# Kernel tuning notes

Measured on AMD Instinct MI355X. Metric: run time of the kernel, lower is better.

The kernel has to match this reference:

```python
import jax, jax.numpy as jnp
import numpy as np

N_NODES = 50000
N_EDGES = 800000
D_IN = 128
D_OUT = 128  # hidden_size == output_size == 128


def setup_inputs() -> dict:
    key = jax.random.key(0)
    k_x, k_src, k_dst, k_w1, k_w2 = jax.random.split(key, 5)
    x = jax.random.normal(k_x, (N_NODES, D_IN), dtype=jnp.float32)
    src = jax.random.randint(k_src, (N_EDGES,), 0, N_NODES)
    dst = jax.random.randint(k_dst, (N_EDGES,), 0, N_NODES)
    # SGConv fc weight (torch Linear layout: [out, in]) and bias
    w_conv = jax.random.normal(k_w1, (D_OUT, D_IN), dtype=jnp.float32) / np.sqrt(D_IN)
    b_conv = jnp.zeros((D_OUT,), dtype=jnp.float32)
    # trailing Linear(hidden_size=128 -> output_size=128)
    w_lin = jax.random.normal(k_w2, (D_OUT, D_OUT), dtype=jnp.float32) / np.sqrt(D_OUT)
    b_lin = jnp.zeros((D_OUT,), dtype=jnp.float32)
    return {"x": x, "src": src, "dst": dst,
            "w_conv": w_conv, "b_conv": b_conv,
            "w_lin": w_lin, "b_lin": b_lin}


def reference(x, src, dst, w_conv, b_conv, w_lin, b_lin):
    n = x.shape[0]
    # symmetric normalization by in-degree (DGL SGConv, k=1 hop)
    deg = jax.ops.segment_sum(jnp.ones_like(dst, dtype=x.dtype), dst, num_segments=n)
    norm = jax.lax.rsqrt(jnp.clip(deg, 1.0))[:, None]  # [N,1]
    h = x * norm                                        # D^{-1/2} X
    h = jax.ops.segment_sum(h[src], dst, num_segments=n)  # A (D^{-1/2} X), spmm via gather+scatter-add
    h = h * norm                                        # D^{-1/2} A D^{-1/2} X
    h = jnp.maximum(h @ w_conv.T + b_conv, 0.0)         # SGConv fc + relu
    return jnp.maximum(h @ w_lin.T + b_lin, 0.0)        # Linear + relu
```

## Files before the change

### kernel.cpp

```cpp
#include <hip/hip_runtime.h>

#define N_NODES 50000
#define N_EDGES 800000
#define D 128
#define ROWS 16
#define BCAP 255
#define LCAP 64
#define ESC_BLOCKS 3125
#define XCONV_BLOCKS 3125
#define NORM_BLOCKS 196
#define WSPLIT_BLOCKS 128
#define XB_OFF 200064
#define WHI_OFF 13000064
#define WS_NEEDED 13131136ull

typedef int   v4i __attribute__((ext_vector_type(4)));
typedef float v4f __attribute__((ext_vector_type(4)));


__device__ __forceinline__ unsigned short bf_rne(float v) {
    unsigned u = __float_as_uint(v);
    u += 0x7FFFu + ((u >> 16) & 1u);
    return (unsigned short)(u >> 16);
}
__device__ __forceinline__ float bf_up(unsigned short h) {
    return __uint_as_float((unsigned)h << 16);
}
__device__ __forceinline__ void split_pack(float a, float b, unsigned& hw, unsigned& lw) {
    unsigned short ha = bf_rne(a);
    unsigned short hb = bf_rne(b);
    unsigned short la = bf_rne(a - bf_up(ha));
    unsigned short lb = bf_rne(b - bf_up(hb));
    hw = (unsigned)ha | ((unsigned)hb << 16);
    lw = (unsigned)la | ((unsigned)lb << 16);
}
__device__ __forceinline__ unsigned pack2(float a, float b) {
    return (unsigned)bf_rne(a) | ((unsigned)bf_rne(b) << 16);
}

__global__ void scatter_kernel(const int* __restrict__ src, const int* __restrict__ dst,
                               int* __restrict__ deg, unsigned short* outSlots,
                               const float* __restrict__ x, unsigned short* __restrict__ xb,
                               const float* __restrict__ w1, const float* __restrict__ w2,
                               unsigned short* __restrict__ whi1, unsigned short* __restrict__ wlo1,
                               unsigned short* __restrict__ whi2, unsigned short* __restrict__ wlo2) {
    int b = blockIdx.x, t = threadIdx.x;
    if (b < ESC_BLOCKS) {
        int e = b * 256 + t;
        int s = src[e], d = dst[e];
        int p = atomicAdd(&deg[d], 1);
        if (p < BCAP) outSlots[(size_t)d * 256 + p] = (unsigned short)s;
    } else if (b < ESC_BLOCKS + XCONV_BLOCKS) {
        int i = (b - ESC_BLOCKS) * 256 + t;
        float4 a = *(const float4*)(x + (size_t)8 * i);
        float4 c = *(const float4*)(x + (size_t)8 * i + 4);
        uint4 o;
        o.x = pack2(a.x, a.y);
        o.y = pack2(a.z, a.w);
        o.z = pack2(c.x, c.y);
        o.w = pack2(c.z, c.w);
        *(uint4*)(xb + (size_t)8 * i) = o;
    } else {
        int m = (b - ESC_BLOCKS - XCONV_BLOCKS) * 256 + t;
        int sel = m >> 14;
        int j = m & 16383;
        float v = sel ? w2[j] : w1[j];
        unsigned short h = bf_rne(v);
        unsigned short lo = bf_rne(v - bf_up(h));
        if (sel) { whi2[j] = h; wlo2[j] = lo; }
        else     { whi1[j] = h; wlo1[j] = lo; }
    }
}

__global__ void prep_kernel(const int* __restrict__ deg, float* __restrict__ normArr,
                            const float* __restrict__ w1, const float* __restrict__ w2,
                            unsigned short* __restrict__ whi1, unsigned short* __restrict__ wlo1,
                            unsigned short* __restrict__ whi2, unsigned short* __restrict__ wlo2) {
    int b = blockIdx.x, t = threadIdx.x;
    if (b < NORM_BLOCKS) {
        int n = b * 256 + t;
        if (n < N_NODES)
            normArr[n] = rsqrtf(fmaxf((float)deg[n], 1.0f));
    } else {
        int m = (b - NORM_BLOCKS) * 256 + t;
        int sel = m >> 14;
        int j = m & 16383;
        float v = sel ? w2[j] : w1[j];
        unsigned short h = bf_rne(v);
        unsigned short lo = bf_rne(v - bf_up(h));
        if (sel) { whi2[j] = h; wlo2[j] = lo; }
        else     { whi1[j] = h; wlo1[j] = lo; }
    }
}

#define MLP_BODY                                                               \
    int wv = t >> 6;                                                           \
    int cb = wv << 5;                                                          \
    int l15 = l & 15;                                                          \
    int kq = l >> 4;                                                           \
    const char* phiA = (const char*)&Ahi[l15][0];                              \
    const char* ploA = (const char*)&Alo[l15][0];                              \
    v4i ahi[4], alo[4];                                                        \
_Pragma("unroll")                                                              \
    for (int kt = 0; kt < 4; ++kt) {                                           \
        int off = ((((kt << 2) | kq) ^ l15) << 4);                             \
        ahi[kt] = *(const v4i*)(phiA + off);                                   \
        alo[kt] = *(const v4i*)(ploA + off);                                   \
    }                                                                          \
    __syncthreads();                                                           \
_Pragma("unroll")                                                              \
    for (int ct = 0; ct < 2; ++ct) {                                           \
        int c = cb + (ct << 4) + l15;                                          \
        float bv = b1[c];                                                      \
        v4f acc = {bv, bv, bv, bv};                                            \
        const unsigned short* wh = whi1 + c * D + (kq << 3);                   \
        const unsigned short* wl = wlo1 + c * D + (kq << 3);                   \
_Pragma("unroll")                                                              \
        for (int kt = 0; kt < 4; ++kt) {                                       \
            v4i bh = *(const v4i*)(wh + (kt << 5));                            \
            v4i bl = *(const v4i*)(wl + (kt << 5));                            \
            asm volatile("v_mfma_f32_16x16x32_bf16 %0, %1, %2, %0" : "+v"(acc) : "v"(ahi[kt]), "v"(bh)); \
            asm volatile("v_mfma_f32_16x16x32_bf16 %0, %1, %2, %0" : "+v"(acc) : "v"(alo[kt]), "v"(bh)); \
            asm volatile("v_mfma_f32_16x16x32_bf16 %0, %1, %2, %0" : "+v"(acc) : "v"(ahi[kt]), "v"(bl)); \
        }                                                                      \
        asm volatile("s_nop 7\n\ts_nop 7" : "+v"(acc));                        \
_Pragma("unroll")                                                              \
        for (int r = 0; r < 4; ++r) {                                          \
            float v = fmaxf(acc[r], 0.0f);                                     \
            unsigned short hv = bf_rne(v);                                     \
            unsigned short lv = bf_rne(v - bf_up(hv));                         \
            int ro = (kq << 2) + r;                                            \
            int byte = (2 * c) ^ ((ro & 15) << 4);                             \
            *(unsigned short*)((char*)&Ahi[ro][0] + byte) = hv;                \
            *(unsigned short*)((char*)&Alo[ro][0] + byte) = lv;                \
        }                                                                      \
    }                                                                          \
    __syncthreads();                                                           \
_Pragma("unroll")                                                              \
    for (int kt = 0; kt < 4; ++kt) {                                           \
        int off = ((((kt << 2) | kq) ^ l15) << 4);                             \
        ahi[kt] = *(const v4i*)(phiA + off);                                   \
        alo[kt] = *(const v4i*)(ploA + off);                                   \
    }                                                                          \
_Pragma("unroll")                                                              \
    for (int ct = 0; ct < 2; ++ct) {                                           \
        int c = cb + (ct << 4) + l15;                                          \
        float bv = b2[c];                                                      \
        v4f acc = {bv, bv, bv, bv};                                            \
        const unsigned short* wh = whi2 + c * D + (kq << 3);                   \
        const unsigned short* wl = wlo2 + c * D + (kq << 3);                   \
_Pragma("unroll")                                                              \
        for (int kt = 0; kt < 4; ++kt) {                                       \
            v4i bh = *(const v4i*)(wh + (kt << 5));                            \
            v4i bl = *(const v4i*)(wl + (kt << 5));                            \
            asm volatile("v_mfma_f32_16x16x32_bf16 %0, %1, %2, %0" : "+v"(acc) : "v"(ahi[kt]), "v"(bh)); \
            asm volatile("v_mfma_f32_16x16x32_bf16 %0, %1, %2, %0" : "+v"(acc) : "v"(alo[kt]), "v"(bh)); \
            asm volatile("v_mfma_f32_16x16x32_bf16 %0, %1, %2, %0" : "+v"(acc) : "v"(ahi[kt]), "v"(bl)); \
        }                                                                      \
        asm volatile("s_nop 7\n\ts_nop 7" : "+v"(acc));                        \
_Pragma("unroll")                                                              \
        for (int r = 0; r < 4; ++r) {                                          \
            int ro = row_base + (kq << 2) + r;                                 \
            if (ro < N_NODES)                                                  \
                io[(size_t)ro * D + c] = fmaxf(acc[r], 0.0f);                  \
        }                                                                      \
    }

__global__ __launch_bounds__(256) void fused_gather_mlp_bf16(
    const unsigned short* __restrict__ xb,
    const unsigned short* slotsIn,
    const int* __restrict__ deg,
    float* io,
    const unsigned short* __restrict__ whi1, const unsigned short* __restrict__ wlo1,
    const float* __restrict__ b1,
    const unsigned short* __restrict__ whi2, const unsigned short* __restrict__ wlo2,
    const float* __restrict__ b2) {
    __shared__ __align__(16) unsigned short Ahi[ROWS][D];
    __shared__ __align__(16) unsigned short Alo[ROWS][D];
    __shared__ unsigned short colsL[ROWS][LCAP];
    __shared__ float ncolL[ROWS][LCAP];
    __shared__ int degL[ROWS];
    __shared__ int nextRow;
    int row_base = blockIdx.x * ROWS;
    int t = threadIdx.x;
    int tx = t & 31;
    int l = t & 63;

    if (t < ROWS) degL[t] = deg[row_base + t];
    if (t == ROWS) nextRow = 0;
    __syncthreads();

    for (int e2 = t; e2 < ROWS * LCAP; e2 += 256) {
        int r = e2 >> 6;
        int j = e2 & (LCAP - 1);
        if (j < degL[r]) {
            int s = slotsIn[(size_t)(row_base + r) * 256 + j];
            colsL[r][j] = (unsigned short)s;
            ncolL[r][j] = rsqrtf(fmaxf((float)deg[s], 1.0f));
        } else {
            colsL[r][j] = 0;
            ncolL[r][j] = 0.f;
        }
    }
    __syncthreads();

    for (;;) {
        int rr;
        if (tx == 0) rr = atomicAdd(&nextRow, 1);
        rr = __shfl(rr, l & 32);
        if (rr >= ROWS) break;
        int dr = degL[rr];
        float nr = rsqrtf(fmaxf((float)dr, 1.0f));
        float4 acc = make_float4(0.f, 0.f, 0.f, 0.f);
        int jend = min(dr, LCAP);
        for (int j = 0; j < jend; j += 8) {
            int s0 = colsL[rr][j + 0], s1 = colsL[rr][j + 1], s2 = colsL[rr][j + 2], s3 = colsL[rr][j + 3];
            int s4 = colsL[rr][j + 4], s5 = colsL[rr][j + 5], s6 = colsL[rr][j + 6], s7 = colsL[rr][j + 7];
            float n0 = ncolL[rr][j + 0], n1 = ncolL[rr][j + 1], n2 = ncolL[rr][j + 2], n3 = ncolL[rr][j + 3];
            float n4 = ncolL[rr][j + 4], n5 = ncolL[rr][j + 5], n6 = ncolL[rr][j + 6], n7 = ncolL[rr][j + 7];
            uint2 v0 = *(const uint2*)(xb + (size_t)s0 * D + 4 * tx);
            uint2 v1 = *(const uint2*)(xb + (size_t)s1 * D + 4 * tx);
            uint2 v2 = *(const uint2*)(xb + (size_t)s2 * D + 4 * tx);
            uint2 v3 = *(const uint2*)(xb + (size_t)s3 * D + 4 * tx);
            uint2 v4 = *(const uint2*)(xb + (size_t)s4 * D + 4 * tx);
            uint2 v5 = *(const uint2*)(xb + (size_t)s5 * D + 4 * tx);
            uint2 v6 = *(const uint2*)(xb + (size_t)s6 * D + 4 * tx);
            uint2 v7 = *(const uint2*)(xb + (size_t)s7 * D + 4 * tx);
            acc.x += __uint_as_float(v0.x << 16) * n0 + __uint_as_float(v1.x << 16) * n1
                   + __uint_as_float(v2.x << 16) * n2 + __uint_as_float(v3.x << 16) * n3
                   + __uint_as_float(v4.x << 16) * n4 + __uint_as_float(v5.x << 16) * n5
                   + __uint_as_float(v6.x << 16) * n6 + __uint_as_float(v7.x << 16) * n7;
            acc.y += __uint_as_float(v0.x & 0xffff0000u) * n0 + __uint_as_float(v1.x & 0xffff0000u) * n1
                   + __uint_as_float(v2.x & 0xffff0000u) * n2 + __uint_as_float(v3.x & 0xffff0000u) * n3
                   + __uint_as_float(v4.x & 0xffff0000u) * n4 + __uint_as_float(v5.x & 0xffff0000u) * n5
                   + __uint_as_float(v6.x & 0xffff0000u) * n6 + __uint_as_float(v7.x & 0xffff0000u) * n7;
            acc.z += __uint_as_float(v0.y << 16) * n0 + __uint_as_float(v1.y << 16) * n1
                   + __uint_as_float(v2.y << 16) * n2 + __uint_as_float(v3.y << 16) * n3
                   + __uint_as_float(v4.y << 16) * n4 + __uint_as_float(v5.y << 16) * n5
                   + __uint_as_float(v6.y << 16) * n6 + __uint_as_float(v7.y << 16) * n7;
            acc.w += __uint_as_float(v0.y & 0xffff0000u) * n0 + __uint_as_float(v1.y & 0xffff0000u) * n1
                   + __uint_as_float(v2.y & 0xffff0000u) * n2 + __uint_as_float(v3.y & 0xffff0000u) * n3
                   + __uint_as_float(v4.y & 0xffff0000u) * n4 + __uint_as_float(v5.y & 0xffff0000u) * n5
                   + __uint_as_float(v6.y & 0xffff0000u) * n6 + __uint_as_float(v7.y & 0xffff0000u) * n7;
        }
        if (dr > LCAP) {
            int je = min(dr, BCAP);
            for (int j = LCAP; j < je; ++j) {
                int s = slotsIn[(size_t)(row_base + rr) * 256 + j];
                float nv = rsqrtf(fmaxf((float)deg[s], 1.0f));
                uint2 v = *(const uint2*)(xb + (size_t)s * D + 4 * tx);
                acc.x += __uint_as_float(v.x << 16) * nv;
                acc.y += __uint_as_float(v.x & 0xffff0000u) * nv;
                acc.z += __uint_as_float(v.y << 16) * nv;
                acc.w += __uint_as_float(v.y & 0xffff0000u) * nv;
            }
        }
        acc.x *= nr; acc.y *= nr; acc.z *= nr; acc.w *= nr;
        unsigned hw0, lw0, hw1, lw1;
        split_pack(acc.x, acc.y, hw0, lw0);
        split_pack(acc.z, acc.w, hw1, lw1);
        int byte = (8 * tx) ^ ((rr & 15) << 4);
        *(uint2*)((char*)&Ahi[rr][0] + byte) = make_uint2(hw0, hw1);
        *(uint2*)((char*)&Alo[rr][0] + byte) = make_uint2(lw0, lw1);
    }
    __syncthreads();

    MLP_BODY
}

__global__ __launch_bounds__(256) void fused_gather_mlp_f32(
    const float* __restrict__ x,
    const unsigned short* slotsIn,
    const float* __restrict__ normArr, const int* __restrict__ deg,
    float* io,
    const unsigned short* __restrict__ whi1, const unsigned short* __restrict__ wlo1,
    const float* __restrict__ b1,
    const unsigned short* __restrict__ whi2, const unsigned short* __restrict__ wlo2,
    const float* __restrict__ b2) {
    __shared__ __align__(16) unsigned short Ahi[ROWS][D];
    __shared__ __align__(16) unsigned short Alo[ROWS][D];
    __shared__ unsigned short colsL[ROWS][LCAP];
    __shared__ float ncolL[ROWS][LCAP];
    __shared__ int degL[ROWS];
    __shared__ int nextRow;
    int row_base = blockIdx.x * ROWS;
    int t = threadIdx.x;
    int tx = t & 31;
    int l = t & 63;

    if (t < ROWS) degL[t] = deg[row_base + t];
    if (t == ROWS) nextRow = 0;
    __syncthreads();

    for (int e2 = t; e2 < ROWS * LCAP; e2 += 256) {
        int r = e2 >> 6;
        int j = e2 & (LCAP - 1);
        if (j < degL[r]) {
            int s = slotsIn[(size_t)(row_base + r) * 256 + j];
            colsL[r][j] = (unsigned short)s;
            ncolL[r][j] = normArr[s];
        } else {
            colsL[r][j] = 0;
            ncolL[r][j] = 0.f;
        }
    }
    __syncthreads();

    for (;;) {
        int rr;
        if (tx == 0) rr = atomicAdd(&nextRow, 1);
        rr = __shfl(rr, l & 32);
        if (rr >= ROWS) break;
        int dr = degL[rr];
        float nr = rsqrtf(fmaxf((float)dr, 1.0f));
        float4 acc = make_float4(0.f, 0.f, 0.f, 0.f);
        int jend = min(dr, LCAP);
        for (int j = 0; j < jend; j += 8) {
            int s0 = colsL[rr][j + 0], s1 = colsL[rr][j + 1], s2 = colsL[rr][j + 2], s3 = colsL[rr][j + 3];
            int s4 = colsL[rr][j + 4], s5 = colsL[rr][j + 5], s6 = colsL[rr][j + 6], s7 = colsL[rr][j + 7];
            float n0 = ncolL[rr][j + 0], n1 = ncolL[rr][j + 1], n2 = ncolL[rr][j + 2], n3 = ncolL[rr][j + 3];
            float n4 = ncolL[rr][j + 4], n5 = ncolL[rr][j + 5], n6 = ncolL[rr][j + 6], n7 = ncolL[rr][j + 7];
            float4 x0 = *(const float4*)(x + (size_t)s0 * D + 4 * tx);
            float4 x1 = *(const float4*)(x + (size_t)s1 * D + 4 * tx);
            float4 x2 = *(const float4*)(x + (size_t)s2 * D + 4 * tx);
            float4 x3 = *(const float4*)(x + (size_t)s3 * D + 4 * tx);
            float4 x4 = *(const float4*)(x + (size_t)s4 * D + 4 * tx);
            float4 x5 = *(const float4*)(x + (size_t)s5 * D + 4 * tx);
            float4 x6 = *(const float4*)(x + (size_t)s6 * D + 4 * tx);
            float4 x7 = *(const float4*)(x + (size_t)s7 * D + 4 * tx);
            acc.x += x0.x * n0 + x1.x * n1 + x2.x * n2 + x3.x * n3
                   + x4.x * n4 + x5.x * n5 + x6.x * n6 + x7.x * n7;
            acc.y += x0.y * n0 + x1.y * n1 + x2.y * n2 + x3.y * n3
                   + x4.y * n4 + x5.y * n5 + x6.y * n6 + x7.y * n7;
            acc.z += x0.z * n0 + x1.z * n1 + x2.z * n2 + x3.z * n3
                   + x4.z * n4 + x5.z * n5 + x6.z * n6 + x7.z * n7;
            acc.w += x0.w * n0 + x1.w * n1 + x2.w * n2 + x3.w * n3
                   + x4.w * n4 + x5.w * n5 + x6.w * n6 + x7.w * n7;
        }
        if (dr > LCAP) {
            int je = min(dr, BCAP);
            for (int j = LCAP; j < je; ++j) {
                int s = slotsIn[(size_t)(row_base + rr) * 256 + j];
                float nv = normArr[s];
                float4 xv = *(const float4*)(x + (size_t)s * D + 4 * tx);
                acc.x += xv.x * nv; acc.y += xv.y * nv;
                acc.z += xv.z * nv; acc.w += xv.w * nv;
            }
        }
        acc.x *= nr; acc.y *= nr; acc.z *= nr; acc.w *= nr;
        unsigned hw0, lw0, hw1, lw1;
        split_pack(acc.x, acc.y, hw0, lw0);
        split_pack(acc.z, acc.w, hw1, lw1);
        int byte = (8 * tx) ^ ((rr & 15) << 4);
        *(uint2*)((char*)&Ahi[rr][0] + byte) = make_uint2(hw0, hw1);
        *(uint2*)((char*)&Alo[rr][0] + byte) = make_uint2(lw0, lw1);
    }
    __syncthreads();

    MLP_BODY
}

extern "C" void kernel_launch(void* const* d_in, const int* in_sizes, int n_in,
                              void* d_out, int out_size, void* d_ws, size_t ws_size,
                              hipStream_t stream) {
    const float* x      = (const float*)d_in[0];
    const int*   src    = (const int*)d_in[1];
    int*         dstbuf = (int*)d_in[2];
    const float* w_conv = (const float*)d_in[3];
    const float* b_conv = (const float*)d_in[4];
    const float* w_lin  = (const float*)d_in[5];
    const float* b_lin  = (const float*)d_in[6];

    int* deg = (int*)d_ws;
    unsigned short* xb = (unsigned short*)((char*)d_ws + XB_OFF);
    const bool big = ws_size >= WS_NEEDED;

    hipMemsetAsync(deg, 0, (size_t)N_NODES * sizeof(int), stream);
    if (big) {
        unsigned short* whi1 = (unsigned short*)((char*)d_ws + WHI_OFF);
        unsigned short* wlo1 = (unsigned short*)((char*)d_ws + WHI_OFF + 32768);
        unsigned short* whi2 = (unsigned short*)((char*)d_ws + WHI_OFF + 65536);
        unsigned short* wlo2 = (unsigned short*)((char*)d_ws + WHI_OFF + 98304);
        scatter_kernel<<<ESC_BLOCKS + XCONV_BLOCKS + WSPLIT_BLOCKS, 256, 0, stream>>>(
            src, (const int*)dstbuf, deg, (unsigned short*)d_out, x, xb,
            w_conv, w_lin, whi1, wlo1, whi2, wlo2);
        fused_gather_mlp_bf16<<<N_NODES / ROWS, 256, 0, stream>>>(
            xb, (const unsigned short*)d_out, deg, (float*)d_out,
            whi1, wlo1, b_conv, whi2, wlo2, b_lin);
    } else {
        float* normArr = (float*)dstbuf;
        unsigned short* whi1 = (unsigned short*)((char*)dstbuf + 200000);
        unsigned short* wlo1 = (unsigned short*)((char*)dstbuf + 232768);
        unsigned short* whi2 = (unsigned short*)((char*)dstbuf + 265536);
        unsigned short* wlo2 = (unsigned short*)((char*)dstbuf + 298304);
        scatter_kernel<<<ESC_BLOCKS, 256, 0, stream>>>(
            src, (const int*)dstbuf, deg, (unsigned short*)d_out, x, xb,
            w_conv, w_lin, whi1, wlo1, whi2, wlo2);
        prep_kernel<<<NORM_BLOCKS + WSPLIT_BLOCKS, 256, 0, stream>>>(
            deg, normArr, w_conv, w_lin, whi1, wlo1, whi2, wlo2);
        fused_gather_mlp_f32<<<N_NODES / ROWS, 256, 0, stream>>>(
            x, (const unsigned short*)d_out, normArr, deg, (float*)d_out,
            whi1, wlo1, b_conv, whi2, wlo2, b_lin);
    }
}
```

Baseline: 204.6 us.

## Replicate degree counters eightfold to reduce atomic contention in edge scatter

Adds a new path, used when the workspace is large enough, that splits each node's degree counter into 8 sub-counters chosen by edge index. Each sub-counter owns a 32-slot region of the node's slot list, which cuts atomic contention on hot destination nodes. The fused gather kernel then sums the sub-counters to get true degrees and compacts the slot lists into shared memory. The costs are an 8x larger memset, extra loads of 8 ints per neighbor for normalization, and more complex slot compaction. Sub-bucket overflow past 32 could also drop edges on skewed inputs.

```diff
diff --git a/kernel.cpp b/kernel.cpp
--- a/kernel.cpp
+++ b/kernel.cpp
@@ -5,6 +5,7 @@
 #define D 128
 #define ROWS 16
 #define BCAP 255
+#define RCAP 32
 #define LCAP 64
 #define ESC_BLOCKS 3125
 #define XCONV_BLOCKS 3125
@@ -12,7 +13,10 @@
 #define WSPLIT_BLOCKS 128
 #define XB_OFF 200064
 #define WHI_OFF 13000064
-#define WS_NEEDED 13131136ull
+#define WS1_NEEDED 13131136ull
+#define XB2_OFF 1600064
+#define WHI2_OFF 14400064
+#define WS2_NEEDED 14531136ull
 
 typedef int   v4i __attribute__((ext_vector_type(4)));
 typedef float v4f __attribute__((ext_vector_type(4)));
@@ -36,6 +40,41 @@
 }
 __device__ __forceinline__ unsigned pack2(float a, float b) {
     return (unsigned)bf_rne(a) | ((unsigned)bf_rne(b) << 16);
+}
+
+__global__ void scatter8_kernel(const int* __restrict__ src, const int* __restrict__ dst,
+                                int* __restrict__ deg8, unsigned short* outSlots,
+                                const float* __restrict__ x, unsigned short* __restrict__ xb,
+                                const float* __restrict__ w1, const float* __restrict__ w2,
+                                unsigned short* __restrict__ whi1, unsigned short* __restrict__ wlo1,
+                                unsigned short* __restrict__ whi2, unsigned short* __restrict__ wlo2) {
+    int b = blockIdx.x, t = threadIdx.x;
+    if (b < ESC_BLOCKS) {
+        int e = b * 256 + t;
+        int s = src[e], d = dst[e];
+        int k = e & 7;
+        int p = atomicAdd(&deg8[(size_t)d * 8 + k], 1);
+        if (p < RCAP) outSlots[(size_t)d * 256 + k * RCAP + p] = (unsigned short)s;
+    } else if (b < ESC_BLOCKS + XCONV_BLOCKS) {
+        int i = (b - ESC_BLOCKS) * 256 + t;
+        float4 a = *(const float4*)(x + (size_t)8 * i);
+        float4 c = *(const float4*)(x + (size_t)8 * i + 4);
+        uint4 o;
+        o.x = pack2(a.x, a.y);
+        o.y = pack2(a.z, a.w);
+        o.z = pack2(c.x, c.y);
+        o.w = pack2(c.z, c.w);
+        *(uint4*)(xb + (size_t)8 * i) = o;
+    } else {
+        int m = (b - ESC_BLOCKS - XCONV_BLOCKS) * 256 + t;
+        int sel = m >> 14;
+        int j = m & 16383;
+        float v = sel ? w2[j] : w1[j];
+        unsigned short h = bf_rne(v);
+        unsigned short lo = bf_rne(v - bf_up(h));
+        if (sel) { whi2[j] = h; wlo2[j] = lo; }
+        else     { whi1[j] = h; wlo1[j] = lo; }
+    }
 }
 
 __global__ void scatter_kernel(const int* __restrict__ src, const int* __restrict__ dst,
@@ -166,6 +205,139 @@
         }                                                                      \
     }
 
+#define BF16_CHUNK8(RR, J)                                                     \
+    {                                                                          \
+        int s0 = colsL[RR][J + 0], s1 = colsL[RR][J + 1], s2 = colsL[RR][J + 2], s3 = colsL[RR][J + 3]; \
+        int s4 = colsL[RR][J + 4], s5 = colsL[RR][J + 5], s6 = colsL[RR][J + 6], s7 = colsL[RR][J + 7]; \
+        float n0 = ncolL[RR][J + 0], n1 = ncolL[RR][J + 1], n2 = ncolL[RR][J + 2], n3 = ncolL[RR][J + 3]; \
+        float n4 = ncolL[RR][J + 4], n5 = ncolL[RR][J + 5], n6 = ncolL[RR][J + 6], n7 = ncolL[RR][J + 7]; \
+        uint2 v0 = *(const uint2*)(xb + (size_t)s0 * D + 4 * tx);              \
+        uint2 v1 = *(const uint2*)(xb + (size_t)s1 * D + 4 * tx);              \
+        uint2 v2 = *(const uint2*)(xb + (size_t)s2 * D + 4 * tx);              \
+        uint2 v3 = *(const uint2*)(xb + (size_t)s3 * D + 4 * tx);              \
+        uint2 v4 = *(const uint2*)(xb + (size_t)s4 * D + 4 * tx);              \
+        uint2 v5 = *(const uint2*)(xb + (size_t)s5 * D + 4 * tx);              \
+        uint2 v6 = *(const uint2*)(xb + (size_t)s6 * D + 4 * tx);              \
+        uint2 v7 = *(const uint2*)(xb + (size_t)s7 * D + 4 * tx);              \
+        acc.x += __uint_as_float(v0.x << 16) * n0 + __uint_as_float(v1.x << 16) * n1 \
+               + __uint_as_float(v2.x << 16) * n2 + __uint_as_float(v3.x << 16) * n3 \
+               + __uint_as_float(v4.x << 16) * n4 + __uint_as_float(v5.x << 16) * n5 \
+               + __uint_as_float(v6.x << 16) * n6 + __uint_as_float(v7.x << 16) * n7; \
+        acc.y += __uint_as_float(v0.x & 0xffff0000u) * n0 + __uint_as_float(v1.x & 0xffff0000u) * n1 \
+               + __uint_as_float(v2.x & 0xffff0000u) * n2 + __uint_as_float(v3.x & 0xffff0000u) * n3 \
+               + __uint_as_float(v4.x & 0xffff0000u) * n4 + __uint_as_float(v5.x & 0xffff0000u) * n5 \
+               + __uint_as_float(v6.x & 0xffff0000u) * n6 + __uint_as_float(v7.x & 0xffff0000u) * n7; \
+        acc.z += __uint_as_float(v0.y << 16) * n0 + __uint_as_float(v1.y << 16) * n1 \
+               + __uint_as_float(v2.y << 16) * n2 + __uint_as_float(v3.y << 16) * n3 \
+               + __uint_as_float(v4.y << 16) * n4 + __uint_as_float(v5.y << 16) * n5 \
+               + __uint_as_float(v6.y << 16) * n6 + __uint_as_float(v7.y << 16) * n7; \
+        acc.w += __uint_as_float(v0.y & 0xffff0000u) * n0 + __uint_as_float(v1.y & 0xffff0000u) * n1 \
+               + __uint_as_float(v2.y & 0xffff0000u) * n2 + __uint_as_float(v3.y & 0xffff0000u) * n3 \
+               + __uint_as_float(v4.y & 0xffff0000u) * n4 + __uint_as_float(v5.y & 0xffff0000u) * n5 \
+               + __uint_as_float(v6.y & 0xffff0000u) * n6 + __uint_as_float(v7.y & 0xffff0000u) * n7; \
+    }
+
+__global__ __launch_bounds__(256) void fused_gather_mlp_rep(
+    const unsigned short* __restrict__ xb,
+    const unsigned short* slotsIn,
+    const int* __restrict__ deg8,
+    float* io,
+    const unsigned short* __restrict__ whi1, const unsigned short* __restrict__ wlo1,
+    const float* __restrict__ b1,
+    const unsigned short* __restrict__ whi2, const unsigned short* __restrict__ wlo2,
+    const float* __restrict__ b2) {
+    __shared__ __align__(16) unsigned short Ahi[ROWS][D];
+    __shared__ __align__(16) unsigned short Alo[ROWS][D];
+    __shared__ unsigned short colsL[ROWS][LCAP];
+    __shared__ float ncolL[ROWS][LCAP];
+    __shared__ unsigned char cntL[ROWS][8];
+    __shared__ unsigned char offL[ROWS][8];
+    __shared__ int dcapL[ROWS];
+    __shared__ float nrL[ROWS];
+    __shared__ int nextRow;
+    int row_base = blockIdx.x * ROWS;
+    int t = threadIdx.x;
+    int tx = t & 31;
+    int l = t & 63;
+
+    for (int i = t; i < ROWS * LCAP; i += 256) {
+        colsL[i >> 6][i & (LCAP - 1)] = 0;
+        ncolL[i >> 6][i & (LCAP - 1)] = 0.f;
+    }
+    if (t == 0) nextRow = 0;
+    if (t < ROWS) {
+        const int4* p = (const int4*)(deg8 + (size_t)(row_base + t) * 8);
+        int4 a = p[0], b = p[1];
+        int cc[8] = {a.x, a.y, a.z, a.w, b.x, b.y, b.z, b.w};
+        int tru = 0, off = 0;
+#pragma unroll
+        for (int k = 0; k < 8; ++k) {
+            tru += cc[k];
+            int c = min(cc[k], RCAP);
+            cntL[t][k] = (unsigned char)c;
+            offL[t][k] = (unsigned char)off;
+            off += c;
+        }
+        dcapL[t] = off;
+        nrL[t] = rsqrtf(fmaxf((float)tru, 1.0f));
+    }
+    __syncthreads();
+
+    for (int e2 = t; e2 < ROWS * 256; e2 += 256) {
+        int r = e2 >> 8, slot = e2 & 255, k = slot >> 5, j = slot & 31;
+        if (j < (int)cntL[r][k]) {
+            int s = slotsIn[(size_t)(row_base + r) * 256 + slot];
+            int idx = (int)offL[r][k] + j;
+            if (idx < LCAP) {
+                colsL[r][idx] = (unsigned short)s;
+                const int4* q = (const int4*)(deg8 + (size_t)s * 8);
+                int4 a = q[0], b = q[1];
+                int sd = a.x + a.y + a.z + a.w + b.x + b.y + b.z + b.w;
+                ncolL[r][idx] = rsqrtf(fmaxf((float)sd, 1.0f));
+            }
+        }
+    }
+    __syncthreads();
+
+    for (;;) {
+        int rr;
+        if (tx == 0) rr = atomicAdd(&nextRow, 1);
+        rr = __shfl(rr, l & 32);
+        if (rr >= ROWS) break;
+        float nr = nrL[rr];
+        float4 acc = make_float4(0.f, 0.f, 0.f, 0.f);
+        int jend = min(dcapL[rr], LCAP);
+        for (int j = 0; j < jend; j += 8) BF16_CHUNK8(rr, j)
+        if (dcapL[rr] > LCAP) {
+            for (int slot = 0; slot < 256; ++slot) {
+                int k = slot >> 5, j = slot & 31;
+                if (j < (int)cntL[rr][k] && (int)offL[rr][k] + j >= LCAP) {
+                    int s = slotsIn[(size_t)(row_base + rr) * 256 + slot];
+                    const int4* q = (const int4*)(deg8 + (size_t)s * 8);
+                    int4 a = q[0], b = q[1];
+                    int sd = a.x + a.y + a.z + a.w + b.x + b.y + b.z + b.w;
+                    float nv = rsqrtf(fmaxf((float)sd, 1.0f));
+                    uint2 v = *(const uint2*)(xb + (size_t)s * D + 4 * tx);
+                    acc.x += __uint_as_float(v.x << 16) * nv;
+                    acc.y += __uint_as_float(v.x & 0xffff0000u) * nv;
+                    acc.z += __uint_as_float(v.y << 16) * nv;
+                    acc.w += __uint_as_float(v.y & 0xffff0000u) * nv;
+                }
+            }
+        }
+        acc.x *= nr; acc.y *= nr; acc.z *= nr; acc.w *= nr;
+        unsigned hw0, lw0, hw1, lw1;
+        split_pack(acc.x, acc.y, hw0, lw0);
+        split_pack(acc.z, acc.w, hw1, lw1);
+        int byte = (8 * tx) ^ ((rr & 15) << 4);
+        *(uint2*)((char*)&Ahi[rr][0] + byte) = make_uint2(hw0, hw1);
+        *(uint2*)((char*)&Alo[rr][0] + byte) = make_uint2(lw0, lw1);
+    }
+    __syncthreads();
+
+    MLP_BODY
+}
+
 __global__ __launch_bounds__(256) void fused_gather_mlp_bf16(
     const unsigned short* __restrict__ xb,
     const unsigned short* slotsIn,
@@ -213,36 +385,7 @@
         float nr = rsqrtf(fmaxf((float)dr, 1.0f));
         float4 acc = make_float4(0.f, 0.f, 0.f, 0.f);
         int jend = min(dr, LCAP);
-        for (int j = 0; j < jend; j += 8) {
-            int s0 = colsL[rr][j + 0], s1 = colsL[rr][j + 1], s2 = colsL[rr][j + 2], s3 = colsL[rr][j + 3];
-            int s4 = colsL[rr][j + 4], s5 = colsL[rr][j + 5], s6 = colsL[rr][j + 6], s7 = colsL[rr][j + 7];
-            float n0 = ncolL[rr][j + 0], n1 = ncolL[rr][j + 1], n2 = ncolL[rr][j + 2], n3 = ncolL[rr][j + 3];
-            float n4 = ncolL[rr][j + 4], n5 = ncolL[rr][j + 5], n6 = ncolL[rr][j + 6], n7 = ncolL[rr][j + 7];
-            uint2 v0 = *(const uint2*)(xb + (size_t)s0 * D + 4 * tx);
-            uint2 v1 = *(const uint2*)(xb + (size_t)s1 * D + 4 * tx);
-            uint2 v2 = *(const uint2*)(xb + (size_t)s2 * D + 4 * tx);
-            uint2 v3 = *(const uint2*)(xb + (size_t)s3 * D + 4 * tx);
-            uint2 v4 = *(const uint2*)(xb + (size_t)s4 * D + 4 * tx);
-            uint2 v5 = *(const uint2*)(xb + (size_t)s5 * D + 4 * tx);
-            uint2 v6 = *(const uint2*)(xb + (size_t)s6 * D + 4 * tx);
-            uint2 v7 = *(const uint2*)(xb + (size_t)s7 * D + 4 * tx);
-            acc.x += __uint_as_float(v0.x << 16) * n0 + __uint_as_float(v1.x << 16) * n1
-                   + __uint_as_float(v2.x << 16) * n2 + __uint_as_float(v3.x << 16) * n3
-                   + __uint_as_float(v4.x << 16) * n4 + __uint_as_float(v5.x << 16) * n5
-                   + __uint_as_float(v6.x << 16) * n6 + __uint_as_float(v7.x << 16) * n7;
-            acc.y += __uint_as_float(v0.x & 0xffff0000u) * n0 + __uint_as_float(v1.x & 0xffff0000u) * n1
-                   + __uint_as_float(v2.x & 0xffff0000u) * n2 + __uint_as_float(v3.x & 0xffff0000u) * n3
-                   + __uint_as_float(v4.x & 0xffff0000u) * n4 + __uint_as_float(v5.x & 0xffff0000u) * n5
-                   + __uint_as_float(v6.x & 0xffff0000u) * n6 + __uint_as_float(v7.x & 0xffff0000u) * n7;
-            acc.z += __uint_as_float(v0.y << 16) * n0 + __uint_as_float(v1.y << 16) * n1
-                   + __uint_as_float(v2.y << 16) * n2 + __uint_as_float(v3.y << 16) * n3
-                   + __uint_as_float(v4.y << 16) * n4 + __uint_as_float(v5.y << 16) * n5
-                   + __uint_as_float(v6.y << 16) * n6 + __uint_as_float(v7.y << 16) * n7;
-            acc.w += __uint_as_float(v0.y & 0xffff0000u) * n0 + __uint_as_float(v1.y & 0xffff0000u) * n1
-                   + __uint_as_float(v2.y & 0xffff0000u) * n2 + __uint_as_float(v3.y & 0xffff0000u) * n3
-                   + __uint_as_float(v4.y & 0xffff0000u) * n4 + __uint_as_float(v5.y & 0xffff0000u) * n5
-                   + __uint_as_float(v6.y & 0xffff0000u) * n6 + __uint_as_float(v7.y & 0xffff0000u) * n7;
-        }
+        for (int j = 0; j < jend; j += 8) BF16_CHUNK8(rr, j)
         if (dr > LCAP) {
             int je = min(dr, BCAP);
             for (int j = LCAP; j < je; ++j) {
@@ -371,16 +514,28 @@
     const float* w_lin  = (const float*)d_in[5];
     const float* b_lin  = (const float*)d_in[6];
 
-    int* deg = (int*)d_ws;
-    unsigned short* xb = (unsigned short*)((char*)d_ws + XB_OFF);
-    const bool big = ws_size >= WS_NEEDED;
-
-    hipMemsetAsync(deg, 0, (size_t)N_NODES * sizeof(int), stream);
-    if (big) {
+    if (ws_size >= WS2_NEEDED) {
+        int* deg8 = (int*)d_ws;
+        unsigned short* xb = (unsigned short*)((char*)d_ws + XB2_OFF);
+        unsigned short* whi1 = (unsigned short*)((char*)d_ws + WHI2_OFF);
+        unsigned short* wlo1 = (unsigned short*)((char*)d_ws + WHI2_OFF + 32768);
+        unsigned short* whi2 = (unsigned short*)((char*)d_ws + WHI2_OFF + 65536);
+        unsigned short* wlo2 = (unsigned short*)((char*)d_ws + WHI2_OFF + 98304);
+        hipMemsetAsync(deg8, 0, (size_t)N_NODES * 8 * sizeof(int), stream);
+        scatter8_kernel<<<ESC_BLOCKS + XCONV_BLOCKS + WSPLIT_BLOCKS, 256, 0, stream>>>(
+            src, (const int*)dstbuf, deg8, (unsigned short*)d_out, x, xb,
+            w_conv, w_lin, whi1, wlo1, whi2, wlo2);
+        fused_gather_mlp_rep<<<N_NODES / ROWS, 256, 0, stream>>>(
+            xb, (const unsigned short*)d_out, deg8, (float*)d_out,
+            whi1, wlo1, b_conv, whi2, wlo2, b_lin);
+    } else if (ws_size >= WS1_NEEDED) {
+        int* deg = (int*)d_ws;
+        unsigned short* xb = (unsigned short*)((char*)d_ws + XB_OFF);
         unsigned short* whi1 = (unsigned short*)((char*)d_ws + WHI_OFF);
         unsigned short* wlo1 = (unsigned short*)((char*)d_ws + WHI_OFF + 32768);
         unsigned short* whi2 = (unsigned short*)((char*)d_ws + WHI_OFF + 65536);
         unsigned short* wlo2 = (unsigned short*)((char*)d_ws + WHI_OFF + 98304);
+        hipMemsetAsync(deg, 0, (size_t)N_NODES * sizeof(int), stream);
         scatter_kernel<<<ESC_BLOCKS + XCONV_BLOCKS + WSPLIT_BLOCKS, 256, 0, stream>>>(
             src, (const int*)dstbuf, deg, (unsigned short*)d_out, x, xb,
             w_conv, w_lin, whi1, wlo1, whi2, wlo2);
@@ -388,13 +543,15 @@
             xb, (const unsigned short*)d_out, deg, (float*)d_out,
             whi1, wlo1, b_conv, whi2, wlo2, b_lin);
     } else {
+        int* deg = (int*)d_ws;
         float* normArr = (float*)dstbuf;
         unsigned short* whi1 = (unsigned short*)((char*)dstbuf + 200000);
         unsigned short* wlo1 = (unsigned short*)((char*)dstbuf + 232768);
         unsigned short* whi2 = (unsigned short*)((char*)dstbuf + 265536);
         unsigned short* wlo2 = (unsigned short*)((char*)dstbuf + 298304);
+        hipMemsetAsync(deg, 0, (size_t)N_NODES * sizeof(int), stream);
         scatter_kernel<<<ESC_BLOCKS, 256, 0, stream>>>(
-            src, (const int*)dstbuf, deg, (unsigned short*)d_out, x, xb,
+            src, (const int*)dstbuf, deg, (unsigned short*)d_out, x, (unsigned short*)d_ws,
             w_conv, w_lin, whi1, wlo1, whi2, wlo2);
         prep_kernel<<<NORM_BLOCKS + WSPLIT_BLOCKS, 256, 0, stream>>>(
             deg, normArr, w_conv, w_lin, whi1, wlo1, whi2, wlo2);
```

After: 224.1 us. +9.5%, slower.
